# Kernel optimization log

Measured on AMD Instinct MI355X. Metric: run time of the kernel, lower is better.

Reference implementation:

```python
import jax, jax.numpy as jnp
import numpy as np

N_COMS = 8
THRESHOLD = 1.0


def setup_inputs() -> dict:
    key = jax.random.key(0)
    k1, k2 = jax.random.split(key)
    N, D, F = 100000, 256, 256
    x = jax.random.normal(k1, (N, F), dtype=jnp.float32)
    z = jax.random.normal(k2, (N, D), dtype=jnp.float32)
    return {"x": x, "z": z}


def reference(x, z):
    N, D = z.shape
    C = N_COMS
    # phi[:, i] = mean of i-th equal chunk of z along features (tensor_split with D % C == 0)
    phi = z.reshape(N, C, D // C).mean(axis=-1)            # [N, C]
    phi = jax.nn.softmax(phi, axis=0)                      # column-wise softmax over nodes

    # chunk_computer, algebraically identical to the masked NxCxCxN einsum:
    # m_1[n,c] = phi[n,c] * sum_{l>n} r[l];  m_2[n,c] = phi[n,c] * sum_{i<n} r[i]
    # => node_weight = phi * (sum(r) - r)[:, None], with r = rowsum(phi)
    r = phi.sum(axis=1)                                    # [N]
    node_weight = phi * (r.sum() - r)[:, None]             # [N, C]

    max_value = node_weight.max(axis=1, keepdims=True)     # [N, 1]
    node_mask = (node_weight == max_value) | (node_weight >= THRESHOLD)  # [N, C] bool

    # x_commun_list: per community, x zeroed outside masked nodes -> stacked [C, N, F]
    x_parts = jnp.where(node_mask.T[:, :, None], x[None, :, :], jnp.zeros((), x.dtype))
    return x_parts, node_mask
```

## Files before the change

### kernel.cpp

```cpp
#include <hip/hip_runtime.h>
#include <cstdint>
#include <cmath>

#define NN 100000
#define NC 8
#define NF 256
#define XPARTS_FLOATS ((size_t)NC * NN * NF)
#define PLANE_VEC ((size_t)NN * 64)
#define CHUNK_ROWS 32
#define NCHUNK (NN / CHUNK_ROWS)

typedef float f32x4 __attribute__((ext_vector_type(4)));

__global__ __launch_bounds__(256) void k_phi_raw(const f32x4* __restrict__ z4,
                                                 double* __restrict__ raw) {
    int gid = blockIdx.x * 256 + threadIdx.x;
    int n = gid >> 6;
    int l = gid & 63;
    if (n >= NN) return;
    f32x4 v = z4[(size_t)n * 64 + l];
    double s = ((double)v.x + (double)v.y) + ((double)v.z + (double)v.w);
    s += __shfl_xor(s, 1, 64);
    s += __shfl_xor(s, 2, 64);
    s += __shfl_xor(s, 4, 64);
    if ((l & 7) == 0) raw[(size_t)n * NC + (l >> 3)] = s * (1.0 / 32.0);
}

__global__ __launch_bounds__(256) void k_col_partial(const double* __restrict__ raw,
                                                     double* __restrict__ part) {
    __shared__ double ss[256][NC];
    int tid = threadIdx.x;
    int gtid = blockIdx.x * 256 + tid;
    double s[NC];
#pragma unroll
    for (int c = 0; c < NC; ++c) s[c] = 0.0;
    for (int n = gtid; n < NN; n += 256 * 256) {
        const double* rp = raw + (size_t)n * NC;
#pragma unroll
        for (int c = 0; c < NC; ++c) s[c] += exp(rp[c]);
    }
#pragma unroll
    for (int c = 0; c < NC; ++c) ss[tid][c] = s[c];
    __syncthreads();
    for (int off = 128; off > 0; off >>= 1) {
        if (tid < off) {
#pragma unroll
            for (int c = 0; c < NC; ++c) ss[tid][c] += ss[tid + off][c];
        }
        __syncthreads();
    }
    if (tid == 0) {
#pragma unroll
        for (int c = 0; c < NC; ++c) part[(size_t)blockIdx.x * NC + c] = ss[0][c];
    }
}

__global__ __launch_bounds__(256) void k_col_final(const double* __restrict__ part,
                                                   double* __restrict__ fin) {
    __shared__ double ss[256][NC];
    int tid = threadIdx.x;
#pragma unroll
    for (int c = 0; c < NC; ++c) ss[tid][c] = part[(size_t)tid * NC + c];
    __syncthreads();
    for (int off = 128; off > 0; off >>= 1) {
        if (tid < off) {
#pragma unroll
            for (int c = 0; c < NC; ++c) ss[tid][c] += ss[tid + off][c];
        }
        __syncthreads();
    }
    if (tid == 0) {
#pragma unroll
        for (int c = 0; c < NC; ++c) fin[c] = ss[0][c];
    }
}

__global__ __launch_bounds__(256) void k_mask(const double* __restrict__ raw,
                                              const double* __restrict__ fin,
                                              float* __restrict__ mask_out) {
    int n = blockIdx.x * blockDim.x + threadIdx.x;
    if (n >= NN) return;
    double phi[NC];
    double r = 0.0;
#pragma unroll
    for (int c = 0; c < NC; ++c) {
        phi[c] = exp(raw[(size_t)n * NC + c]) / fin[c];
        r += phi[c];
    }
    double f = 8.0 - r;
    double w[NC];
    double wmax = -1e300;
#pragma unroll
    for (int c = 0; c < NC; ++c) { w[c] = phi[c] * f; wmax = fmax(wmax, w[c]); }
#pragma unroll
    for (int c = 0; c < NC; ++c) {
        bool bit = (w[c] == wmax) || (w[c] >= 1.0);
        mask_out[(size_t)n * NC + c] = bit ? 1.0f : 0.0f;
    }
}

__global__ __launch_bounds__(256) void k_scatter_lin(
    const f32x4* __restrict__ x4, const float* __restrict__ mask,
    f32x4* __restrict__ out4) {
    int bid = blockIdx.x;
    int c = bid & 7;
    int chunk = bid >> 3;
    int r0 = chunk * CHUNK_ROWS;
    size_t base = (size_t)r0 * 64;
    __shared__ float bits[CHUNK_ROWS];
    int tid = threadIdx.x;
    if (tid < CHUNK_ROWS) bits[tid] = mask[(size_t)(r0 + tid) * NC + c];
    __syncthreads();
    const f32x4 zz = (f32x4)(0.f);
    size_t obase = (size_t)c * PLANE_VEC + base;
#pragma unroll
    for (int i = 0; i < 8; ++i) {
        int idx = i * 256 + tid;
        f32x4 v = x4[base + idx];
        bool bit = bits[idx >> 6] != 0.0f;
        __builtin_nontemporal_store(bit ? v : zz, &out4[obase + idx]);
    }
}

extern "C" void kernel_launch(void* const* d_in, const int* in_sizes, int n_in,
                              void* d_out, int out_size, void* d_ws, size_t ws_size,
                              hipStream_t stream) {
    const f32x4* x4 = (const f32x4*)d_in[0];
    const f32x4* z4 = (const f32x4*)d_in[1];
    float* out = (float*)d_out;
    float* mask_out = out + XPARTS_FLOATS;

    const size_t RAW_BYTES  = (size_t)NN * NC * sizeof(double);
    const size_t PART_BYTES = 256 * NC * sizeof(double);
    const size_t FIN_BYTES  = NC * sizeof(double);

    double *raw, *part, *fin;
    if (ws_size >= RAW_BYTES + PART_BYTES + FIN_BYTES) {
        raw  = (double*)d_ws;
        part = (double*)((char*)d_ws + RAW_BYTES);
        fin  = (double*)((char*)d_ws + RAW_BYTES + PART_BYTES);
    } else {
        raw  = (double*)out;
        part = (double*)(out + 2000000);
        fin  = (double*)(out + 2200000);
    }

    k_phi_raw    <<<(NN * 64 + 255) / 256, 256, 0, stream>>>(z4, raw);
    k_col_partial<<<256, 256, 0, stream>>>(raw, part);
    k_col_final  <<<1, 256, 0, stream>>>(part, fin);
    k_mask       <<<(NN + 255) / 256, 256, 0, stream>>>(raw, fin, mask_out);
    k_scatter_lin<<<NCHUNK * NC, 256, 0, stream>>>(x4, mask_out, (f32x4*)out);
}
```

Measured before the change: 223.7 us.

## Split scatter into zero-fill and single-read multi-plane copy kernels

Replaces the per-community scatter kernel, which read x once for each of the 8 communities, with two kernels. One writes zeros to the unmasked rows of each plane, and one reads each x row once and stores it into every plane whose mask bit is set. This cuts x reads from 8 passes to 1 and keeps the total write volume the same. The cost is an extra kernel launch, with the copy's stores spread across planes in a less linear pattern.

Measured after the change: 196.2 us (median of 2 runs). 12.3% less time.

```diff
diff --git a/kernel.cpp b/kernel.cpp
--- a/kernel.cpp
+++ b/kernel.cpp
@@ -99,26 +99,42 @@
     }
 }
 
-__global__ __launch_bounds__(256) void k_scatter_lin(
-    const f32x4* __restrict__ x4, const float* __restrict__ mask,
-    f32x4* __restrict__ out4) {
+__global__ __launch_bounds__(256) void k_fill_holes(const float* __restrict__ mask,
+                                                    f32x4* __restrict__ out4) {
     int bid = blockIdx.x;
-    int c = bid & 7;
-    int chunk = bid >> 3;
+    int c = bid / NCHUNK;
+    int chunk = bid - c * NCHUNK;
     int r0 = chunk * CHUNK_ROWS;
-    size_t base = (size_t)r0 * 64;
+    int tid = threadIdx.x;
     __shared__ float bits[CHUNK_ROWS];
-    int tid = threadIdx.x;
     if (tid < CHUNK_ROWS) bits[tid] = mask[(size_t)(r0 + tid) * NC + c];
     __syncthreads();
+    size_t obase = (size_t)c * PLANE_VEC + (size_t)r0 * 64;
     const f32x4 zz = (f32x4)(0.f);
-    size_t obase = (size_t)c * PLANE_VEC + base;
 #pragma unroll
-    for (int i = 0; i < 8; ++i) {
+    for (int i = 0; i < (CHUNK_ROWS * 64) / 256; ++i) {
         int idx = i * 256 + tid;
-        f32x4 v = x4[base + idx];
-        bool bit = bits[idx >> 6] != 0.0f;
-        __builtin_nontemporal_store(bit ? v : zz, &out4[obase + idx]);
+        if (bits[idx >> 6] == 0.0f)
+            __builtin_nontemporal_store(zz, &out4[obase + idx]);
+    }
+}
+
+__global__ __launch_bounds__(256) void k_copy(const f32x4* __restrict__ x4,
+                                              const float* __restrict__ mask,
+                                              f32x4* __restrict__ out4) {
+    int gid = blockIdx.x * 256 + threadIdx.x;
+    int n = gid >> 6;
+    int lane = gid & 63;
+    if (n >= NN) return;
+    f32x4 v = x4[(size_t)n * 64 + lane];
+    const f32x4* m4 = (const f32x4*)(mask + (size_t)n * NC);
+    f32x4 m0 = m4[0], m1 = m4[1];
+    float mm[NC] = {m0.x, m0.y, m0.z, m0.w, m1.x, m1.y, m1.z, m1.w};
+    size_t rbase = (size_t)n * 64 + lane;
+#pragma unroll
+    for (int c = 0; c < NC; ++c) {
+        if (mm[c] != 0.0f)
+            __builtin_nontemporal_store(v, &out4[(size_t)c * PLANE_VEC + rbase]);
     }
 }
 
@@ -149,5 +165,6 @@
     k_col_partial<<<256, 256, 0, stream>>>(raw, part);
     k_col_final  <<<1, 256, 0, stream>>>(part, fin);
     k_mask       <<<(NN + 255) / 256, 256, 0, stream>>>(raw, fin, mask_out);
-    k_scatter_lin<<<NCHUNK * NC, 256, 0, stream>>>(x4, mask_out, (f32x4*)out);
+    k_fill_holes <<<NC * NCHUNK, 256, 0, stream>>>(mask_out, (f32x4*)out);
+    k_copy       <<<(NN * 64) / 256, 256, 0, stream>>>(x4, mask_out, (f32x4*)out);
 }
```
